# Performance work log

Measured on AMD Instinct MI355X. Metric: run time of the kernel, lower is better.

## Reference

```python
import jax, jax.numpy as jnp
import numpy as np

J = 7
Q = 12
T = 16000
STRIDE = 2 ** J            # subsample factor 128 -> 125 output samples
EPS_N = 1e-8
EPS_L = 1e-5
ALPHA = 0.7


def _filters():
    """Analytic Morlet-like filter bank in the Fourier domain (fixed constants)."""
    omega = np.arange(T, dtype=np.float64) / T          # normalized freq in [0,1)
    # first-order wavelets: Q per octave over J octaves -> J*Q filters
    xi1 = 0.5 * 2.0 ** (-(np.arange(J * Q) + 1.0) / Q)  # center freqs [P1]
    sig1 = xi1 * (2.0 ** (1.0 / Q) - 1.0) * 2.0
    psi1 = np.exp(-((omega[None, :] - xi1[:, None]) ** 2) / (2.0 * sig1[:, None] ** 2))
    # second-order wavelets: one per octave -> J filters
    xi2 = 0.5 * 2.0 ** (-(np.arange(J) + 1.0))
    sig2 = xi2 * 0.5
    psi2 = np.exp(-((omega[None, :] - xi2[:, None]) ** 2) / (2.0 * sig2[:, None] ** 2))
    # lowpass phi matched to 2^J subsampling; symmetric so lowpassed real stays real
    sig_phi = 0.4 / STRIDE
    phi = (np.exp(-(omega ** 2) / (2.0 * sig_phi ** 2))
           + np.exp(-((omega - 1.0) ** 2) / (2.0 * sig_phi ** 2)))
    # valid second-order paths: octave of psi2 strictly deeper than octave of psi1
    j1 = np.arange(J * Q) // Q                           # octave index of each psi1
    i1, i2 = np.nonzero(j1[:, None] < np.arange(J)[None, :])
    return (jnp.asarray(psi1, jnp.float32), jnp.asarray(psi2, jnp.float32),
            jnp.asarray(phi, jnp.float32), i1, i2)

PSI1, PSI2, PHI, I1, I2 = _filters()   # C = 1 + 84 + 252 = 337 channels


def setup_inputs() -> dict:
    key = jax.random.key(0)
    x = jax.random.normal(key, (8, T), dtype=jnp.float32)
    return {"x": x}


def _scatter(x):
    # Hann-based tapering window (0.92*hann + 0.08), periodic like torch.hann_window
    n = jnp.arange(T, dtype=x.dtype)
    window = 0.92 * (0.5 * (1.0 - jnp.cos(2.0 * jnp.pi * n / T))) + 0.08
    x = x * window[None, :]                                  # [B, T]
    X = jnp.fft.fft(x)                                       # [B, T] complex
    # order 0: lowpass + subsample
    S0 = jnp.fft.ifft(X * PHI).real[:, ::STRIDE][:, None, :]  # [B, 1, 125]
    # order 1: |x * psi1| then lowpass + subsample
    U1 = jnp.abs(jnp.fft.ifft(X[:, None, :] * PSI1[None, :, :]))  # [B, P1, T]
    U1h = jnp.fft.fft(U1)
    S1 = jnp.fft.ifft(U1h * PHI).real[:, :, ::STRIDE]             # [B, P1, 125]
    # order 2: ||x*psi1| * psi2| along valid (j1, j2) paths, then lowpass
    U2 = jnp.abs(jnp.fft.ifft(U1h[:, I1, :] * PSI2[I2][None, :, :]))  # [B, P, T]
    S2 = jnp.fft.ifft(jnp.fft.fft(U2) * PHI).real[:, :, ::STRIDE]     # [B, P, 125]
    return jnp.concatenate([S0, S1, S2], axis=1)                     # [B, 337, 125]


def reference(x):
    Sx = _scatter(x)
    # eval-mode normalization: channel_mean=0, channel_std=1 buffers
    Sx_n = Sx / (1.0 + EPS_N)
    sign = jnp.sign(Sx_n)
    log_t = sign * jnp.log1p(jnp.abs(Sx_n) / EPS_L) * EPS_L
    return ALPHA * Sx_n + (1.0 - ALPHA) * log_t
```

## Files before the change

kernel.cpp:

```cpp
#include <hip/hip_runtime.h>

#define TN 16000

constexpr int nrad(int L){
  return (L%10==0) ? 10 : (L%5==0) ? 5 : (L>=8 && L!=16) ? 8 : (L>=4) ? 4 : 2;
}

__device__ __forceinline__ float2 cmulf(float2 a, float2 b){
  return make_float2(a.x*b.x - a.y*b.y, a.x*b.y + a.y*b.x);
}
__device__ __forceinline__ float2 cadd(float2 a, float2 b){ return make_float2(a.x+b.x, a.y+b.y); }
__device__ __forceinline__ float2 csub(float2 a, float2 b){ return make_float2(a.x-b.x, a.y-b.y); }

template<int L>
__device__ __forceinline__ int f2p(int k){
  if constexpr (L == 1) return 0;
  else {
    constexpr int R = nrad(L);
    return (k % R) * (L / R) + f2p<L / R>(k / R);
  }
}
template<int L>
__device__ __forceinline__ int p2f(int p){
  if constexpr (L == 1) return 0;
  else {
    constexpr int R = nrad(L);
    const int hi = p / (L / R);
    const int lo = p - hi * (L / R);
    return hi + R * p2f<L / R>(lo);
  }
}

template<bool SWZ>
__device__ __forceinline__ int sx(int i){ return SWZ ? (i ^ ((i >> 7) & 7)) : i; }

template<bool INV>
__device__ __forceinline__ void dft5c(float2* t){
  const float CR[5]={1.f,0.30901699437494742f,-0.80901699437494745f,
                     -0.80901699437494745f,0.30901699437494742f};
  const float CI[5]={0.f,-0.95105651629515357f,-0.58778525229247313f,
                     0.58778525229247313f,0.95105651629515357f};
  float2 y[5];
#pragma unroll
  for (int i=0;i<5;i++) y[i]=t[i];
#pragma unroll
  for (int u=0;u<5;u++){
    float zr=0.f, zi=0.f;
#pragma unroll
    for (int k=0;k<5;k++){
      const int m=(k*u)%5;
      const float wr=CR[m];
      const float wi=INV? -CI[m]:CI[m];
      zr += y[k].x*wr - y[k].y*wi;
      zi += y[k].x*wi + y[k].y*wr;
    }
    t[u]=make_float2(zr,zi);
  }
}

template<bool INV>
__device__ __forceinline__ void dft4c(float2* a){
  float2 s02=cadd(a[0],a[2]), d02=csub(a[0],a[2]);
  float2 s13=cadd(a[1],a[3]), d13=csub(a[1],a[3]);
  a[0]=cadd(s02,s13); a[2]=csub(s02,s13);
  if constexpr (INV){
    a[1]=make_float2(d02.x-d13.y, d02.y+d13.x);
    a[3]=make_float2(d02.x+d13.y, d02.y-d13.x);
  } else {
    a[1]=make_float2(d02.x+d13.y, d02.y-d13.x);
    a[3]=make_float2(d02.x-d13.y, d02.y+d13.x);
  }
}

template<bool INV>
__device__ __forceinline__ void dft8(float2* y){
  float2 e[4]={y[0],y[2],y[4],y[6]};
  float2 o[4]={y[1],y[3],y[5],y[7]};
  dft4c<INV>(e); dft4c<INV>(o);
  const float C=0.70710678118654752f;
  const float2 w1 = INV ? make_float2(C,C)   : make_float2(C,-C);
  const float2 w2 = INV ? make_float2(0.f,1.f): make_float2(0.f,-1.f);
  const float2 w3 = INV ? make_float2(-C,C)  : make_float2(-C,-C);
  float2 t;
  t=o[0];            y[0]=cadd(e[0],t); y[4]=csub(e[0],t);
  t=cmulf(o[1],w1);  y[1]=cadd(e[1],t); y[5]=csub(e[1],t);
  t=cmulf(o[2],w2);  y[2]=cadd(e[2],t); y[6]=csub(e[2],t);
  t=cmulf(o[3],w3);  y[3]=cadd(e[3],t); y[7]=csub(e[3],t);
}

template<bool INV>
__device__ __forceinline__ void dft10(float2* y){
  float2 e[5]={y[0],y[2],y[4],y[6],y[8]};
  float2 o[5]={y[1],y[3],y[5],y[7],y[9]};
  dft5c<INV>(e); dft5c<INV>(o);
  const float CR[5]={1.f,0.80901699437494745f,0.30901699437494742f,
                     -0.30901699437494742f,-0.80901699437494745f};
  const float SI[5]={0.f,0.58778525229247313f,0.95105651629515357f,
                     0.95105651629515357f,0.58778525229247313f};
#pragma unroll
  for (int u=0;u<5;u++){
    const float2 w = make_float2(CR[u], INV ? SI[u] : -SI[u]);
    const float2 t = cmulf(o[u], w);
    y[u]   = cadd(e[u], t);
    y[u+5] = csub(e[u], t);
  }
}

template<bool INV>
__device__ __forceinline__ float2 w25c(int m){
  const float CR[17]={1.f,0.968583161f,0.876306680f,0.728968627f,0.535826795f,
                      0.309016994f,0.062790520f,-0.187381315f,-0.425779292f,
                      -0.637423990f,-0.809016994f,-0.929776486f,-0.992114701f,
                      -0.992114701f,-0.929776486f,-0.809016994f,-0.637423990f};
  const float SI[17]={0.f,0.248689887f,0.481753674f,0.684547106f,0.844327926f,
                      0.951056516f,0.998026728f,0.982287251f,0.904827052f,
                      0.770513243f,0.587785252f,0.368124553f,0.125333234f,
                      -0.125333234f,-0.368124553f,-0.587785252f,-0.770513243f};
  return make_float2(CR[m], INV ? SI[m] : -SI[m]);
}

template<bool INV>
__device__ __forceinline__ void dft25(float2* y){
  float2 g[25];
#pragma unroll
  for (int a=0;a<5;a++){
    float2 t[5];
#pragma unroll
    for (int b=0;b<5;b++) t[b]=y[a+5*b];
    dft5c<INV>(t);
#pragma unroll
    for (int c=0;c<5;c++){
      float2 v=t[c];
      const int m=a*c;
      if (m) v=cmulf(v, w25c<INV>(m));
      g[a+5*c]=v;
    }
  }
#pragma unroll
  for (int c=0;c<5;c++){
    float2 t[5];
#pragma unroll
    for (int a=0;a<5;a++) t[a]=g[a+5*c];
    dft5c<INV>(t);
#pragma unroll
    for (int d=0;d<5;d++) y[c+5*d]=t[d];
  }
}

template<int R, bool INV>
__device__ __forceinline__ void dftR(float2* y){
  if constexpr (R==2){ float2 a=y[0],b=y[1]; y[0]=cadd(a,b); y[1]=csub(a,b); }
  else if constexpr (R==4){ dft4c<INV>(y); }
  else if constexpr (R==5){ dft5c<INV>(y); }
  else if constexpr (R==8){ dft8<INV>(y); }
  else { dft10<INV>(y); }
}

template<int R, bool INV>
__device__ __forceinline__ void twiddles(float2* y, int j, float invL){
  if (j == 0) return;
  const float ang = (INV ? 6.28318530717958647692f : -6.28318530717958647692f)
                    * (float)j * invL;
  float s,c; __sincosf(ang,&s,&c);
  const float2 w = make_float2(c,s);
  float2 wp = w;
  y[1]=cmulf(y[1],wp);
#pragma unroll
  for (int u=2;u<R;u++){ wp=cmulf(wp,w); y[u]=cmulf(y[u],wp); }
}

template<bool INV>
__device__ __forceinline__ void twiddles25(float2* y, int j, float invL){
  if (j == 0) return;
  const float ang = (INV ? 6.28318530717958647692f : -6.28318530717958647692f)
                    * (float)j * invL;
  float s,c; __sincosf(ang,&s,&c);
  const float2 w1=make_float2(c,s);
  __sincosf(5.f*ang,&s,&c);
  const float2 w5=make_float2(c,s);
  float2 Wb[5], Wa[5];
  Wb[1]=w1; Wb[2]=cmulf(w1,w1); Wb[3]=cmulf(Wb[2],w1); Wb[4]=cmulf(Wb[2],Wb[2]);
  Wa[1]=w5; Wa[2]=cmulf(w5,w5); Wa[3]=cmulf(Wa[2],w5); Wa[4]=cmulf(Wa[2],Wa[2]);
#pragma unroll
  for (int a=0;a<5;a++)
#pragma unroll
    for (int b=0;b<5;b++){
      const int u=5*a+b;
      if (u==0) continue;
      float2 v=y[u];
      if (a) v=cmulf(v,Wa[a]);
      if (b) v=cmulf(v,Wb[b]);
      y[u]=v;
    }
}

template<int N, int L, int R, bool INV, int EPI, bool SWZ>
__device__ void stageg(float2* buf, int tid, int nt, float esc){
  constexpr int M = L/R;
  constexpr float invL = 1.f/(float)L;
  for (int f = tid; f < N/R; f += nt){
    const int blk = f / M;
    const int j = f - blk*M;
    const int base = blk*L + j;
    float2 y[R];
#pragma unroll
    for (int t=0;t<R;t++) y[t]=buf[sx<SWZ>(base + t*M)];
    if constexpr (INV){
      twiddles<R,true>(y,j,invL);
      dftR<R,true>(y);
    } else {
      dftR<R,false>(y);
      twiddles<R,false>(y,j,invL);
    }
#pragma unroll
    for (int u=0;u<R;u++){
      if constexpr (EPI==1)
        buf[sx<SWZ>(base+u*M)]=make_float2(sqrtf(y[u].x*y[u].x+y[u].y*y[u].y)*esc, 0.f);
      else
        buf[sx<SWZ>(base+u*M)]=y[u];
    }
  }
}

template<int N, int L, bool SWZ>
__device__ void fwd_rec(float2* buf, int tid, int nt){
  if constexpr (L > 1){
    constexpr int R = nrad(L);
    stageg<N,L,R,false,0,SWZ>(buf,tid,nt,0.f);
    __syncthreads();
    fwd_rec<N,L/R,SWZ>(buf,tid,nt);
  }
}
template<int N, int L, int EPI, bool SWZ>
__device__ void inv_rec(float2* buf, int tid, int nt, float esc){
  if constexpr (L > 1){
    constexpr int R = nrad(L);
    inv_rec<N,L/R,0,SWZ>(buf,tid,nt,0.f);
    stageg<N,L,R,true,(L==N?EPI:0),SWZ>(buf,tid,nt,esc);
    __syncthreads();
  }
}

__device__ __forceinline__ float norm_val(float s){
  const float lt = log1pf(fabsf(s)*1.0e5f)*1.0e-5f;
  return 0.7f*s + 0.3f*copysignf(lt, s);
}

__global__ __launch_bounds__(256) void k_split(const float* __restrict__ x,
                                               float2* __restrict__ Xmid,
                                               float* __restrict__ out){
  __shared__ float sseg[4384];
  __shared__ float stab[412];
  const int tid = threadIdx.x;
  if (blockIdx.x >= 20){
    const int s = blockIdx.x - 20;
    const int b = s >> 2;
    const int o0 = (s & 3) * 32;
    const float* xb = x + b*TN;
    const int n0 = o0*128 - 204;
    for (int i=tid;i<4377;i+=256){
      int n = n0 + i;
      n += (n < 0) ? TN : 0;
      n -= (n >= TN) ? TN : 0;
      const float c=__cosf((float)n*(6.28318530717958647692f/16000.0f));
      sseg[i]=xb[n]*(0.08f+0.46f*(1.0f-c));
    }
    for (int i=tid;i<409;i+=256){
      const float dd=(float)(i-204);
      stab[i]=0.0078332134f*__expf(-1.9276571e-4f*dd*dd);
    }
    __syncthreads();
    const int o=tid>>3, g=tid&7;
    float acc=0.f;
    for (int d=-204+g; d<=204; d+=8)
      acc += stab[d+204]*sseg[o*128 + 204 - d];
    acc += __shfl_xor(acc,1); acc += __shfl_xor(acc,2); acc += __shfl_xor(acc,4);
    if (g==0 && o0+o<125) out[(size_t)b*337*125 + o0+o]=norm_val(acc);
    return;
  }
  const int gid = blockIdx.x*256 + tid;
  const int b = gid/640, j = gid - (gid/640)*640;
  const float* xb = x + b*TN;
  float2 y[25];
#pragma unroll
  for (int t=0;t<25;t++){
    const int n=j+640*t;
    const float c=__cosf((float)n*(6.28318530717958647692f/16000.0f));
    y[t]=make_float2(xb[n]*(0.08f+0.46f*(1.0f-c)), 0.f);
  }
  dft25<false>(y);
  twiddles25<false>(y, j, 1.f/16000.f);
  float2* Xm = Xmid + (size_t)b*TN;
#pragma unroll
  for (int u=0;u<25;u++) Xm[u*640+j]=y[u];
}

__global__ __launch_bounds__(128) void k_sub(const float2* __restrict__ Xmid,
                                             float2* __restrict__ Xnat){
  __shared__ float2 sb[640];
  const int tid=threadIdx.x;
  const int b=blockIdx.x/25, u0=blockIdx.x%25;
  const float2* src = Xmid + (size_t)b*TN + u0*640;
  for (int i=tid;i<640;i+=128) sb[i]=src[i];
  __syncthreads();
  fwd_rec<640,640,false>(sb,tid,128);
  float2* Xb = Xnat + (size_t)b*TN;
  for (int m=tid;m<640;m+=128) Xb[u0+25*m]=sb[f2p<640>(m)];
}

template<int W, int NT>
__device__ void o1body(const float2* __restrict__ Xnat, float2* __restrict__ U1h,
                       float* __restrict__ out, int b, int p1, int tid,
                       float2* buf, float* htab, int store_n, int zero_to){
  constexpr float TAU = 16000.f/(float)W;
  constexpr int DMAX = (204*W + TN-1)/TN;
  constexpr int OSTEP = W/125;
  for (int i=tid; i<2*DMAX+1; i+=NT){
    const float dd = TAU*(float)(i-DMAX);
    htab[i]=0.0078332134f*__expf(-1.9276571e-4f*dd*dd);
  }
  const float xi = 0.5f*exp2f(-(float)(p1+1)*(1.0f/12.0f));
  const float sg = xi*0.11892618871859045f;
  const float niv = -1.f/(2.f*sg*sg);
  int k0 = (int)(16000.f*(xi+5.f*sg)) + 1 - W;
  if (k0 < 0) k0 = 0;
  const float2* Xb = Xnat + (size_t)b*TN;
  for (int p=tid;p<W;p+=NT){
    const int k = k0 + p2f<W>(p);
    const float d=(float)k*(1.f/16000.f)-xi;
    const float g=__expf(niv*d*d);
    const float2 v=Xb[k];
    buf[sx<true>(p)]=make_float2(v.x*g, v.y*g);
  }
  __syncthreads();
  inv_rec<W,W,1,true>(buf,tid,NT,1.f/16000.f);
  constexpr int G = (NT >= 1024) ? 8 : (NT >= 512) ? 4 : 1;
  {
    const int o = (G>1) ? (tid/G) : tid;
    const int g = (G>1) ? (tid%G) : 0;
    float acc=0.f;
    if (o<125){
      for (int d=-DMAX+g; d<=DMAX; d+=G){
        int ix=o*OSTEP-d;
        ix += (ix<0)?W:0; ix -= (ix>=W)?W:0;
        acc += htab[d+DMAX]*buf[sx<true>(ix)].x;
      }
    }
    if constexpr (G==8){ acc += __shfl_xor(acc,1); acc += __shfl_xor(acc,2); acc += __shfl_xor(acc,4); }
    else if constexpr (G==4){ acc += __shfl_xor(acc,1); acc += __shfl_xor(acc,2); }
    if (o<125 && g==0) out[((size_t)b*337+1+p1)*125+o]=norm_val(TAU*acc);
  }
  if (store_n>0){
    __syncthreads();
    fwd_rec<W,W,true>(buf,tid,NT);
    float2* Ub = U1h + (size_t)(b*84+p1)*8000;
    for (int k=tid;k<store_n;k+=NT){
      const float2 v=buf[sx<true>(f2p<W>(k))];
      Ub[k]=make_float2(TAU*v.x, TAU*v.y);
    }
    for (int k=store_n+tid;k<zero_to;k+=NT) Ub[k]=make_float2(0.f,0.f);
  }
}

__global__ __launch_bounds__(1024) void k_order1(const float2* __restrict__ Xnat,
                                                 float2* __restrict__ U1h,
                                                 float* __restrict__ out){
  __shared__ float2 buf[10000];
  __shared__ float htab[257];
  const int tid=threadIdx.x;
  const int a=blockIdx.x/96, r=blockIdx.x%96, b=r/12, idx=r%12;
  const int p1=a*12+idx;
  switch(a){
    case 0: o1body<10000,1024>(Xnat,U1h,out,b,p1,tid,buf,htab,8000,8000); break;
    case 1: o1body< 5000,1024>(Xnat,U1h,out,b,p1,tid,buf,htab,4000,4000); break;
    case 2: o1body< 2500,1024>(Xnat,U1h,out,b,p1,tid,buf,htab,2000,2000); break;
    case 3: o1body< 1250,1024>(Xnat,U1h,out,b,p1,tid,buf,htab,1000,1000); break;
    case 4: o1body<  625,1024>(Xnat,U1h,out,b,p1,tid,buf,htab, 625,1000); break;
    case 5: o1body<  500,1024>(Xnat,U1h,out,b,p1,tid,buf,htab, 500, 500); break;
    default: o1body< 250,1024>(Xnat,U1h,out,b,p1,tid,buf,htab,   0,   0); break;
  }
}

template<int N, int NT>
__device__ void o2body(const float2* __restrict__ U1h, float* __restrict__ out,
                       int b, int p1, int j2, int q, int tid,
                       float2* buf, float* htab){
  constexpr int R = TN/N;
  constexpr int CMAX = (204*N + TN-1)/TN;
  constexpr int OSTEP = 128/R;
  for (int i=tid; i<2*CMAX+1; i+=NT){
    const float dd = (float)((i-CMAX)*R);
    htab[i]=0.0078332134f*__expf(-1.9276571e-4f*dd*dd);
  }
  const float xi = 0.5f*exp2f(-(float)(j2+1));
  const float sg = 0.5f*xi;
  const float niv = -1.f/(2.f*sg*sg);
  const float2* Zb = U1h + (size_t)(b*84+p1)*8000;
  for (int p=tid;p<N;p+=NT){
    const int k = p2f<N>(p);
    const float d=(float)k*(1.f/16000.f)-xi;
    const float g=__expf(niv*d*d);
    const float2 v=Zb[k];
    buf[sx<true>(p)]=make_float2(v.x*g, v.y*g);
  }
  __syncthreads();
  inv_rec<N,N,1,true>(buf,tid,NT,1.f/16000.f);
  constexpr int G = (NT >= 512) ? 4 : 1;
  const int o = (G>1) ? (tid/G) : tid;
  const int g = (G>1) ? (tid%G) : 0;
  float acc=0.f;
  if (o<125){
    for (int c=-CMAX+g; c<=CMAX; c+=G){
      int ix=o*OSTEP-c;
      ix += (ix<0)?N:0; ix -= (ix>=N)?N:0;
      acc += htab[c+CMAX]*buf[sx<true>(ix)].x;
    }
  }
  if constexpr (G==4){ acc += __shfl_xor(acc,1); acc += __shfl_xor(acc,2); }
  if (o<125 && g==0) out[((size_t)b*337+85+q)*125+o]=norm_val((float)R*acc);
}

__global__ __launch_bounds__(512,4) void k_order2(const float2* __restrict__ U1h,
                                                  float* __restrict__ out){
  __shared__ float2 buf[8000];
  __shared__ float htab[205];
  const int tid=threadIdx.x;
  int id=blockIdx.x;
  int j2;
  if      (id<  96){ j2=1; }
  else if (id< 288){ j2=2; id-=  96; }
  else if (id< 576){ j2=3; id-= 288; }
  else if (id< 960){ j2=4; id-= 576; }
  else if (id<1440){ j2=5; id-= 960; }
  else             { j2=6; id-=1440; }
  const int npath=12*j2;
  const int b=id/npath, p1=id%npath;
  const int a=p1/12, rr=p1%12;
  const int q=12*(6*a-(a*(a-1))/2)+rr*(6-a)+(j2-a-1);
  switch(j2){
    case 1: o2body<8000,512>(U1h,out,b,p1,1,q,tid,buf,htab); break;
    case 2: o2body<4000,512>(U1h,out,b,p1,2,q,tid,buf,htab); break;
    case 3: o2body<2000,512>(U1h,out,b,p1,3,q,tid,buf,htab); break;
    case 4: o2body<1000,512>(U1h,out,b,p1,4,q,tid,buf,htab); break;
    case 5: o2body<1000,512>(U1h,out,b,p1,5,q,tid,buf,htab); break;
    default: o2body<500,512>(U1h,out,b,p1,6,q,tid,buf,htab); break;
  }
}

extern "C" void kernel_launch(void* const* d_in, const int* in_sizes, int n_in,
                              void* d_out, int out_size, void* d_ws, size_t ws_size,
                              hipStream_t stream){
  (void)in_sizes; (void)n_in; (void)out_size; (void)ws_size;
  const float* x = (const float*)d_in[0];
  float* out = (float*)d_out;
  float2* Xmid = (float2*)d_ws;
  float2* Xnat = (float2*)((char*)d_ws + (size_t)8*TN*sizeof(float2));
  float2* U1h  = (float2*)((char*)d_ws + (size_t)16*TN*sizeof(float2));
  k_split <<<52,   256, 0, stream>>>(x, Xmid, out);
  k_sub   <<<200,  128, 0, stream>>>(Xmid, Xnat);
  k_order1<<<672, 1024, 0, stream>>>(Xnat, U1h, out);
  k_order2<<<2016, 512, 0, stream>>>(U1h, out);
}
```

Measured before the change: 92.81 us.

## Pack several small-size scattering paths into one block for order-1 and order-2

For the smaller FFT sizes in both the order-1 and order-2 kernels, one block now processes 2, 4 or 8 paths at once. Each path gets its own thread subgroup and its own padded shared-memory slice, and the two large sizes keep the single-path bodies. This targets the many mostly idle threads and the high block count that came from giving a whole 1024- or 512-thread block to a transform of a few hundred or thousand points. In exchange, the lowpass dot product drops its per-output thread-group shuffle reduction, so each output is summed by one thread. Subgroups also share block-wide barriers inside the FFT routines.

After: 93.67 us. No clear change (+0.9%).

```diff
diff --git a/kernel.cpp b/kernel.cpp
--- a/kernel.cpp
+++ b/kernel.cpp
@@ -362,22 +362,82 @@
   }
 }
 
+template<int W, int NT, int MP>
+__device__ void o1body_mp(const float2* __restrict__ Xnat, float2* __restrict__ U1h,
+                          float* __restrict__ out, int a, int r0, int tid,
+                          float2* bufall, float* htab, int store_n, int zero_to){
+  constexpr int PT = NT/MP;
+  constexpr int WP = W+8;
+  constexpr float TAU = 16000.f/(float)W;
+  constexpr int DMAX = (204*W + TN-1)/TN;
+  constexpr int OSTEP = W/125;
+  for (int i=tid; i<2*DMAX+1; i+=NT){
+    const float dd = TAU*(float)(i-DMAX);
+    htab[i]=0.0078332134f*__expf(-1.9276571e-4f*dd*dd);
+  }
+  const int sub = tid/PT, lt = tid - sub*PT;
+  const int r = r0 + sub;
+  const int b = r/12, p1 = a*12 + (r%12);
+  float2* buf = bufall + sub*WP;
+  const float xi = 0.5f*exp2f(-(float)(p1+1)*(1.0f/12.0f));
+  const float sg = xi*0.11892618871859045f;
+  const float niv = -1.f/(2.f*sg*sg);
+  int k0 = (int)(16000.f*(xi+5.f*sg)) + 1 - W;
+  if (k0 < 0) k0 = 0;
+  const float2* Xb = Xnat + (size_t)b*TN;
+  for (int p=lt;p<W;p+=PT){
+    const int k = k0 + p2f<W>(p);
+    const float d=(float)k*(1.f/16000.f)-xi;
+    const float g=__expf(niv*d*d);
+    const float2 v=Xb[k];
+    buf[sx<true>(p)]=make_float2(v.x*g, v.y*g);
+  }
+  __syncthreads();
+  inv_rec<W,W,1,true>(buf,lt,PT,1.f/16000.f);
+  for (int o=lt;o<125;o+=PT){
+    float acc=0.f;
+    for (int d=-DMAX; d<=DMAX; ++d){
+      int ix=o*OSTEP-d;
+      ix += (ix<0)?W:0; ix -= (ix>=W)?W:0;
+      acc += htab[d+DMAX]*buf[sx<true>(ix)].x;
+    }
+    out[((size_t)b*337+1+p1)*125+o]=norm_val(TAU*acc);
+  }
+  if (store_n>0){
+    __syncthreads();
+    fwd_rec<W,W,true>(buf,lt,PT);
+    float2* Ub = U1h + (size_t)(b*84+p1)*8000;
+    for (int k=lt;k<store_n;k+=PT){
+      const float2 v=buf[sx<true>(f2p<W>(k))];
+      Ub[k]=make_float2(TAU*v.x, TAU*v.y);
+    }
+    for (int k=store_n+lt;k<zero_to;k+=PT) Ub[k]=make_float2(0.f,0.f);
+  }
+}
+
 __global__ __launch_bounds__(1024) void k_order1(const float2* __restrict__ Xnat,
                                                  float2* __restrict__ U1h,
                                                  float* __restrict__ out){
   __shared__ float2 buf[10000];
   __shared__ float htab[257];
   const int tid=threadIdx.x;
-  const int a=blockIdx.x/96, r=blockIdx.x%96, b=r/12, idx=r%12;
-  const int p1=a*12+idx;
-  switch(a){
-    case 0: o1body<10000,1024>(Xnat,U1h,out,b,p1,tid,buf,htab,8000,8000); break;
-    case 1: o1body< 5000,1024>(Xnat,U1h,out,b,p1,tid,buf,htab,4000,4000); break;
-    case 2: o1body< 2500,1024>(Xnat,U1h,out,b,p1,tid,buf,htab,2000,2000); break;
-    case 3: o1body< 1250,1024>(Xnat,U1h,out,b,p1,tid,buf,htab,1000,1000); break;
-    case 4: o1body<  625,1024>(Xnat,U1h,out,b,p1,tid,buf,htab, 625,1000); break;
-    case 5: o1body<  500,1024>(Xnat,U1h,out,b,p1,tid,buf,htab, 500, 500); break;
-    default: o1body< 250,1024>(Xnat,U1h,out,b,p1,tid,buf,htab,   0,   0); break;
+  const int id=blockIdx.x;
+  if (id < 96){
+    const int r=id, b=r/12, p1=r%12;
+    o1body<10000,1024>(Xnat,U1h,out,b,p1,tid,buf,htab,8000,8000);
+  } else if (id < 192){
+    const int r=id-96, b=r/12, p1=12+(r%12);
+    o1body< 5000,1024>(Xnat,U1h,out,b,p1,tid,buf,htab,4000,4000);
+  } else if (id < 240){
+    o1body_mp<2500,1024,2>(Xnat,U1h,out,2,(id-192)*2,tid,buf,htab,2000,2000);
+  } else if (id < 264){
+    o1body_mp<1250,1024,4>(Xnat,U1h,out,3,(id-240)*4,tid,buf,htab,1000,1000);
+  } else if (id < 288){
+    o1body_mp< 625,1024,4>(Xnat,U1h,out,4,(id-264)*4,tid,buf,htab, 625,1000);
+  } else if (id < 312){
+    o1body_mp< 500,1024,4>(Xnat,U1h,out,5,(id-288)*4,tid,buf,htab, 500, 500);
+  } else {
+    o1body_mp< 250,1024,8>(Xnat,U1h,out,6,(id-312)*8,tid,buf,htab,   0,   0);
   }
 }
 
@@ -420,30 +480,74 @@
   if (o<125 && g==0) out[((size_t)b*337+85+q)*125+o]=norm_val((float)R*acc);
 }
 
+template<int N, int NT, int MP>
+__device__ void o2body_mp(const float2* __restrict__ U1h, float* __restrict__ out,
+                          int j2, int id0, int tid, float2* bufall, float* htab){
+  constexpr int PT = NT/MP;
+  constexpr int NP = N+8;
+  constexpr int R = TN/N;
+  constexpr int CMAX = (204*N + TN-1)/TN;
+  constexpr int OSTEP = 128/R;
+  for (int i=tid; i<2*CMAX+1; i+=NT){
+    const float dd = (float)((i-CMAX)*R);
+    htab[i]=0.0078332134f*__expf(-1.9276571e-4f*dd*dd);
+  }
+  const int sub = tid/PT, lt = tid - sub*PT;
+  const int npath=12*j2;
+  const int id = id0 + sub;
+  const int b=id/npath, p1=id%npath;
+  const int a=p1/12, rr=p1%12;
+  const int q=12*(6*a-(a*(a-1))/2)+rr*(6-a)+(j2-a-1);
+  float2* buf = bufall + sub*NP;
+  const float xi = 0.5f*exp2f(-(float)(j2+1));
+  const float sg = 0.5f*xi;
+  const float niv = -1.f/(2.f*sg*sg);
+  const float2* Zb = U1h + (size_t)(b*84+p1)*8000;
+  for (int p=lt;p<N;p+=PT){
+    const int k = p2f<N>(p);
+    const float d=(float)k*(1.f/16000.f)-xi;
+    const float g=__expf(niv*d*d);
+    const float2 v=Zb[k];
+    buf[sx<true>(p)]=make_float2(v.x*g, v.y*g);
+  }
+  __syncthreads();
+  inv_rec<N,N,1,true>(buf,lt,PT,1.f/16000.f);
+  for (int o=lt;o<125;o+=PT){
+    float acc=0.f;
+    for (int c=-CMAX; c<=CMAX; ++c){
+      int ix=o*OSTEP-c;
+      ix += (ix<0)?N:0; ix -= (ix>=N)?N:0;
+      acc += htab[c+CMAX]*buf[sx<true>(ix)].x;
+    }
+    out[((size_t)b*337+85+q)*125+o]=norm_val((float)R*acc);
+  }
+}
+
 __global__ __launch_bounds__(512,4) void k_order2(const float2* __restrict__ U1h,
                                                   float* __restrict__ out){
   __shared__ float2 buf[8000];
   __shared__ float htab[205];
   const int tid=threadIdx.x;
-  int id=blockIdx.x;
-  int j2;
-  if      (id<  96){ j2=1; }
-  else if (id< 288){ j2=2; id-=  96; }
-  else if (id< 576){ j2=3; id-= 288; }
-  else if (id< 960){ j2=4; id-= 576; }
-  else if (id<1440){ j2=5; id-= 960; }
-  else             { j2=6; id-=1440; }
-  const int npath=12*j2;
-  const int b=id/npath, p1=id%npath;
-  const int a=p1/12, rr=p1%12;
-  const int q=12*(6*a-(a*(a-1))/2)+rr*(6-a)+(j2-a-1);
-  switch(j2){
-    case 1: o2body<8000,512>(U1h,out,b,p1,1,q,tid,buf,htab); break;
-    case 2: o2body<4000,512>(U1h,out,b,p1,2,q,tid,buf,htab); break;
-    case 3: o2body<2000,512>(U1h,out,b,p1,3,q,tid,buf,htab); break;
-    case 4: o2body<1000,512>(U1h,out,b,p1,4,q,tid,buf,htab); break;
-    case 5: o2body<1000,512>(U1h,out,b,p1,5,q,tid,buf,htab); break;
-    default: o2body<500,512>(U1h,out,b,p1,6,q,tid,buf,htab); break;
+  const int id=blockIdx.x;
+  if (id < 96){
+    const int b=id/12, p1=id%12;
+    const int q=(1-0-1)+p1*6;
+    o2body<8000,512>(U1h,out,b,p1,1,q,tid,buf,htab);
+  } else if (id < 288){
+    const int t=id-96;
+    const int npath=24;
+    const int b=t/npath, p1=t%npath;
+    const int a=p1/12, rr=p1%12;
+    const int q=12*(6*a-(a*(a-1))/2)+rr*(6-a)+(2-a-1);
+    o2body<4000,512>(U1h,out,b,p1,2,q,tid,buf,htab);
+  } else if (id < 432){
+    o2body_mp<2000,512,2>(U1h,out,3,(id-288)*2,tid,buf,htab);
+  } else if (id < 528){
+    o2body_mp<1000,512,4>(U1h,out,4,(id-432)*4,tid,buf,htab);
+  } else if (id < 648){
+    o2body_mp<1000,512,4>(U1h,out,5,(id-528)*4,tid,buf,htab);
+  } else {
+    o2body_mp< 500,512,8>(U1h,out,6,(id-648)*8,tid,buf,htab);
   }
 }
 
@@ -458,6 +562,6 @@
   float2* U1h  = (float2*)((char*)d_ws + (size_t)16*TN*sizeof(float2));
   k_split <<<52,   256, 0, stream>>>(x, Xmid, out);
   k_sub   <<<200,  128, 0, stream>>>(Xmid, Xnat);
-  k_order1<<<672, 1024, 0, stream>>>(Xnat, U1h, out);
-  k_order2<<<2016, 512, 0, stream>>>(U1h, out);
-}
+  k_order1<<<324, 1024, 0, stream>>>(Xnat, U1h, out);
+  k_order2<<<720,  512, 0, stream>>>(U1h, out);
+}
```

## Pack multiple small second-order paths per block in order-2 kernel

Applied to the files above, without the earlier changes.

For the shorter FFT lengths (j2>=3), several paths are now processed concurrently in one 512-thread block, each by its own thread subgroup with its own shared buffer slice. This cuts the grid from 2016 to 720 blocks and raises per-thread utilisation for the small transforms, which previously left most threads idle. The launch-bounds occupancy hint is dropped. A single block-wide barrier inside the per-path inverse transform may need care, and the lowpass reduction loses its 4-way thread split.

After: 95.12 us. +2.5%, slower.

```diff
diff --git a/kernel.cpp b/kernel.cpp
--- a/kernel.cpp
+++ b/kernel.cpp
@@ -420,30 +420,74 @@
   if (o<125 && g==0) out[((size_t)b*337+85+q)*125+o]=norm_val((float)R*acc);
 }
 
-__global__ __launch_bounds__(512,4) void k_order2(const float2* __restrict__ U1h,
-                                                  float* __restrict__ out){
+template<int N, int NT, int MP>
+__device__ void o2body_mp(const float2* __restrict__ U1h, float* __restrict__ out,
+                          int j2, int id0, int tid, float2* bufall, float* htab){
+  constexpr int PT = NT/MP;
+  constexpr int NP = N+8;
+  constexpr int R = TN/N;
+  constexpr int CMAX = (204*N + TN-1)/TN;
+  constexpr int OSTEP = 128/R;
+  for (int i=tid; i<2*CMAX+1; i+=NT){
+    const float dd = (float)((i-CMAX)*R);
+    htab[i]=0.0078332134f*__expf(-1.9276571e-4f*dd*dd);
+  }
+  const int sub = tid/PT, lt = tid - sub*PT;
+  const int npath=12*j2;
+  const int id = id0 + sub;
+  const int b=id/npath, p1=id%npath;
+  const int a=p1/12, rr=p1%12;
+  const int q=12*(6*a-(a*(a-1))/2)+rr*(6-a)+(j2-a-1);
+  float2* buf = bufall + sub*NP;
+  const float xi = 0.5f*exp2f(-(float)(j2+1));
+  const float sg = 0.5f*xi;
+  const float niv = -1.f/(2.f*sg*sg);
+  const float2* Zb = U1h + (size_t)(b*84+p1)*8000;
+  for (int p=lt;p<N;p+=PT){
+    const int k = p2f<N>(p);
+    const float d=(float)k*(1.f/16000.f)-xi;
+    const float g=__expf(niv*d*d);
+    const float2 v=Zb[k];
+    buf[sx<true>(p)]=make_float2(v.x*g, v.y*g);
+  }
+  __syncthreads();
+  inv_rec<N,N,1,true>(buf,lt,PT,1.f/16000.f);
+  for (int o=lt;o<125;o+=PT){
+    float acc=0.f;
+    for (int c=-CMAX; c<=CMAX; ++c){
+      int ix=o*OSTEP-c;
+      ix += (ix<0)?N:0; ix -= (ix>=N)?N:0;
+      acc += htab[c+CMAX]*buf[sx<true>(ix)].x;
+    }
+    out[((size_t)b*337+85+q)*125+o]=norm_val((float)R*acc);
+  }
+}
+
+__global__ __launch_bounds__(512) void k_order2(const float2* __restrict__ U1h,
+                                                float* __restrict__ out){
   __shared__ float2 buf[8000];
   __shared__ float htab[205];
   const int tid=threadIdx.x;
-  int id=blockIdx.x;
-  int j2;
-  if      (id<  96){ j2=1; }
-  else if (id< 288){ j2=2; id-=  96; }
-  else if (id< 576){ j2=3; id-= 288; }
-  else if (id< 960){ j2=4; id-= 576; }
-  else if (id<1440){ j2=5; id-= 960; }
-  else             { j2=6; id-=1440; }
-  const int npath=12*j2;
-  const int b=id/npath, p1=id%npath;
-  const int a=p1/12, rr=p1%12;
-  const int q=12*(6*a-(a*(a-1))/2)+rr*(6-a)+(j2-a-1);
-  switch(j2){
-    case 1: o2body<8000,512>(U1h,out,b,p1,1,q,tid,buf,htab); break;
-    case 2: o2body<4000,512>(U1h,out,b,p1,2,q,tid,buf,htab); break;
-    case 3: o2body<2000,512>(U1h,out,b,p1,3,q,tid,buf,htab); break;
-    case 4: o2body<1000,512>(U1h,out,b,p1,4,q,tid,buf,htab); break;
-    case 5: o2body<1000,512>(U1h,out,b,p1,5,q,tid,buf,htab); break;
-    default: o2body<500,512>(U1h,out,b,p1,6,q,tid,buf,htab); break;
+  const int id=blockIdx.x;
+  if (id < 96){
+    const int b=id/12, p1=id%12;
+    const int q=6*p1;
+    o2body<8000,512>(U1h,out,b,p1,1,q,tid,buf,htab);
+  } else if (id < 288){
+    const int t=id-96;
+    const int npath=24;
+    const int b=t/npath, p1=t%npath;
+    const int a=p1/12, rr=p1%12;
+    const int q=12*(6*a-(a*(a-1))/2)+rr*(6-a)+(2-a-1);
+    o2body<4000,512>(U1h,out,b,p1,2,q,tid,buf,htab);
+  } else if (id < 432){
+    o2body_mp<2000,512,2>(U1h,out,3,(id-288)*2,tid,buf,htab);
+  } else if (id < 528){
+    o2body_mp<1000,512,4>(U1h,out,4,(id-432)*4,tid,buf,htab);
+  } else if (id < 648){
+    o2body_mp<1000,512,4>(U1h,out,5,(id-528)*4,tid,buf,htab);
+  } else {
+    o2body_mp< 500,512,8>(U1h,out,6,(id-648)*8,tid,buf,htab);
   }
 }
 
@@ -459,5 +503,5 @@
   k_split <<<52,   256, 0, stream>>>(x, Xmid, out);
   k_sub   <<<200,  128, 0, stream>>>(Xmid, Xnat);
   k_order1<<<672, 1024, 0, stream>>>(Xnat, U1h, out);
-  k_order2<<<2016, 512, 0, stream>>>(U1h, out);
-}
+  k_order2<<<720,  512, 0, stream>>>(U1h, out);
+}
```
